# Performance work log

Measured on AMD Instinct MI355X. Metric: run time of the kernel, lower is better.

## Reference

```python
import jax, jax.numpy as jnp
import numpy as np

N_EMBD = 1024
N_HEAD = 16
HEAD_DIM = N_EMBD // N_HEAD


def setup_inputs() -> dict:
    key = jax.random.key(0)
    ks = jax.random.split(key, 8)
    B, T, T_ctx, C = 2, 2048, 2048, N_EMBD
    s = 1.0 / np.sqrt(C)
    return {
        "x": jax.random.normal(ks[0], (B, T, C), dtype=jnp.float32),
        "context": jax.random.normal(ks[1], (B, T_ctx, C), dtype=jnp.float32),
        # Linear weights stored as [in, out] (torch stores [out, in]; math identical via x @ W)
        "Wq": jax.random.normal(ks[2], (C, C), dtype=jnp.float32) * s,
        "bq": jnp.zeros((C,), dtype=jnp.float32),
        "Wkv": jax.random.normal(ks[3], (C, 2 * C), dtype=jnp.float32) * s,
        "bkv": jnp.zeros((2 * C,), dtype=jnp.float32),
        "Wp": jax.random.normal(ks[4], (C, C), dtype=jnp.float32) * s,
        "bp": jnp.zeros((C,), dtype=jnp.float32),
    }


def reference(x, context, Wq, bq, Wkv, bkv, Wp, bp):
    B, T, C = x.shape
    T_ctx = context.shape[1]
    H, D = N_HEAD, C // N_HEAD

    q = (x @ Wq + bq).reshape(B, T, H, D).transpose(0, 2, 1, 3)          # [B,H,T,D]
    kv = context @ Wkv + bkv                                             # [B,T_ctx,2C]
    k, v = jnp.split(kv, 2, axis=-1)
    k = k.reshape(B, T_ctx, H, D).transpose(0, 2, 1, 3)                  # [B,H,T_ctx,D]
    v = v.reshape(B, T_ctx, H, D).transpose(0, 2, 1, 3)                  # [B,H,T_ctx,D]

    att = jnp.einsum("bhtd,bhsd->bhts", q, k) * (1.0 / jnp.sqrt(jnp.asarray(D, q.dtype)))
    # tril(ones(T, T_ctx)): position t attends to context positions s <= t
    causal = jnp.arange(T)[:, None] >= jnp.arange(T_ctx)[None, :]        # [T,T_ctx]
    att = jnp.where(causal[None, None], att, jnp.asarray(-jnp.inf, att.dtype))
    att = jax.nn.softmax(att, axis=-1)

    y = jnp.einsum("bhts,bhsd->bhtd", att, v)                            # [B,H,T,D]
    y = y.transpose(0, 2, 1, 3).reshape(B, T, C)
    return y @ Wp + bp
```

## Files before the change

### kernel.cpp

```cpp
#include <hip/hip_runtime.h>
#include <hip/hip_bf16.h>

typedef __bf16 bf16;
typedef __bf16 bf16x8 __attribute__((ext_vector_type(8)));
typedef __bf16 bf16x4 __attribute__((ext_vector_type(4)));
typedef float f32x4 __attribute__((ext_vector_type(4)));
typedef float f32x16 __attribute__((ext_vector_type(16)));

#define GLOAD_LDS16(g, l) \
  __builtin_amdgcn_global_load_lds((const __attribute__((address_space(1))) void*)(g), \
                                   (__attribute__((address_space(3))) void*)(l), 16, 0, 0)

static __device__ __forceinline__ unsigned cvtpk_bf16(float lo, float hi) {
  unsigned r;
  asm("v_cvt_pk_bf16_f32 %0, %1, %2" : "=v"(r) : "v"(lo), "v"(hi));
  return r;
}
static __device__ __forceinline__ void pl32swap(unsigned& a, unsigned& b) {
  asm volatile("v_permlane32_swap_b32 %0, %1" : "+v"(a), "+v"(b));
}

__global__ __launch_bounds__(256) void prep_kernel(
    const float* __restrict__ x, const float* __restrict__ ctx,
    const float* __restrict__ Wq, const float* __restrict__ Wkv, const float* __restrict__ Wp,
    bf16* __restrict__ x_bf, bf16* __restrict__ c_bf,
    bf16* __restrict__ Wq_t, bf16* __restrict__ Wkv_t, bf16* __restrict__ Wp_t) {
  const int bid = blockIdx.x;
  const int tid = threadIdx.x;
  if (bid < 8192) {
    const int i = (bid & 4095) * 256 + tid;
    const float4 v = (bid < 4096) ? ((const float4*)x)[i] : ((const float4*)ctx)[i];
    bf16x4 o;
    o.x = (bf16)v.x; o.y = (bf16)v.y; o.z = (bf16)v.z; o.w = (bf16)v.w;
    if (bid < 4096) ((bf16x4*)x_bf)[i] = o; else ((bf16x4*)c_bf)[i] = o;
    return;
  }
  __shared__ float tile[128][33];
  int tb = bid - 8192;
  const float* W; bf16* Wt; int N, by, bx;
  if (tb < 256)       { W = Wq;  Wt = Wq_t;  N = 1024; by = tb >> 5; bx = tb & 31; }
  else if (tb < 768)  { tb -= 256; W = Wkv; Wt = Wkv_t; N = 2048; by = tb >> 6; bx = tb & 63; }
  else                { tb -= 768; W = Wp;  Wt = Wp_t;  N = 1024; by = tb >> 5; bx = tb & 31; }
  const int k0 = by * 128, n0 = bx * 32;
#pragma unroll
  for (int i = 0; i < 16; ++i) {
    const int idx = tid + i * 256;
    const int r = idx >> 5, c = idx & 31;
    tile[r][c] = W[(size_t)(k0 + r) * N + n0 + c];
  }
  __syncthreads();
#pragma unroll
  for (int p = 0; p < 2; ++p) {
    const int slot = tid + p * 256;
    const int n = slot >> 4, kg = slot & 15;
    bf16x8 v;
#pragma unroll
    for (int j = 0; j < 8; ++j) v[j] = (bf16)tile[kg * 8 + j][n];
    *(bf16x8*)(Wt + (size_t)(n0 + n) * 1024 + k0 + kg * 8) = v;
  }
}

__global__ __launch_bounds__(512) void proj_gemm_kernel(
    const bf16* __restrict__ x_bf, const bf16* __restrict__ c_bf,
    const bf16* __restrict__ Wq_t, const bf16* __restrict__ Wkv_t,
    const float* __restrict__ bq, const float* __restrict__ bkv,
    bf16* __restrict__ Qh, bf16* __restrict__ Kh, bf16* __restrict__ Vt) {
  __shared__ __align__(16) bf16 SM[24576];
  bf16* As = SM;
  bf16* Bs = SM + 16384;
  bf16* Vb = SM;

  const int tid = threadIdx.x;
  const int lane = tid & 63;
  const int w = tid >> 6;
  const int wm = w >> 2, wn = w & 3;
  const int g4 = lane >> 4, r16 = lane & 15;
  const int wu = __builtin_amdgcn_readfirstlane(w);

  int bid = blockIdx.x;
  bid = (bid & 7) * 48 + (bid >> 3);
  const bool isq = bid < 128;
  const int lid = isq ? bid : bid - 128;
  const int bx = isq ? (lid & 7) : (lid & 15);
  const int by = isq ? (lid >> 3) : (lid >> 4);
  const int m0 = by * 256, n0 = bx * 128;
  const bf16* A = isq ? x_bf : c_bf;
  const bf16* Bt = isq ? Wq_t : Wkv_t;
  const float* bias = isq ? bq : bkv;

  const bf16* Abase = A + (size_t)m0 * 1024;
  const bf16* Bbase = Bt + (size_t)n0 * 1024;
  int aoff[4], boff[2];
#pragma unroll
  for (int it = 0; it < 4; ++it) {
    const int s = it * 512 + tid;
    const int row = s >> 3, j = s & 7;
    aoff[it] = row * 1024 + (j ^ (row & 7)) * 8;
  }
#pragma unroll
  for (int it = 0; it < 2; ++it) {
    const int s = it * 512 + tid;
    const int row = s >> 3, j = s & 7;
    boff[it] = row * 1024 + (j ^ (row & 7)) * 8;
  }

  f32x4 acc[8][2] = {};

  for (int k0 = 0; k0 < 1024; k0 += 64) {
    __syncthreads();
#pragma unroll
    for (int it = 0; it < 4; ++it)
      GLOAD_LDS16(Abase + aoff[it] + k0, As + (it * 512 + wu * 64) * 8);
#pragma unroll
    for (int it = 0; it < 2; ++it)
      GLOAD_LDS16(Bbase + boff[it] + k0, Bs + (it * 512 + wu * 64) * 8);
    __syncthreads();
#pragma unroll
    for (int kk = 0; kk < 2; ++kk) {
      bf16x8 bfr[2];
#pragma unroll
      for (int ni = 0; ni < 2; ni++) {
        const int lr = wn * 32 + ni * 16 + r16;
        bfr[ni] = *(const bf16x8*)(Bs + lr * 64 + ((kk * 4 + g4) ^ (lr & 7)) * 8);
      }
#pragma unroll
      for (int mi = 0; mi < 8; mi++) {
        const int lr = wm * 128 + mi * 16 + r16;
        const bf16x8 a = *(const bf16x8*)(As + lr * 64 + ((kk * 4 + g4) ^ (lr & 7)) * 8);
        acc[mi][0] = __builtin_amdgcn_mfma_f32_16x16x32_bf16(a, bfr[0], acc[mi][0], 0, 0, 0);
        acc[mi][1] = __builtin_amdgcn_mfma_f32_16x16x32_bf16(a, bfr[1], acc[mi][1], 0, 0, 0);
      }
    }
  }

  if (!isq && n0 >= 1024) {
    const int bb = m0 >> 11, t0l = m0 & 2047;
#pragma unroll
    for (int p = 0; p < 2; ++p) {
      __syncthreads();
      if ((wn >> 1) == p) {
#pragma unroll
        for (int mi = 0; mi < 8; mi++)
#pragma unroll
          for (int ni = 0; ni < 2; ni++) {
            const int cl = (wn & 1) * 32 + ni * 16 + r16;
            const float bv = bias[n0 + p * 64 + cl];
#pragma unroll
            for (int r = 0; r < 4; r++) {
              const int rl = wm * 128 + mi * 16 + 4 * g4 + r;
              Vb[cl * 264 + rl] = (bf16)(acc[mi][ni][r] + bv);
            }
          }
      }
      __syncthreads();
      const int c2b = n0 - 1024 + p * 64;
#pragma unroll
      for (int pp = 0; pp < 4; ++pp) {
        const int slot = tid + pp * 512;
        const int d = slot >> 5, j = slot & 31;
        const int cc = c2b + d;
        const int h = cc >> 6, dd = cc & 63;
        *(bf16x8*)(Vt + ((size_t)((bb * 16 + h) * 64 + dd)) * 2048 + t0l + j * 8) =
            *(const bf16x8*)(Vb + d * 264 + j * 8);
      }
    }
    return;
  }

#pragma unroll
  for (int mi = 0; mi < 8; mi++) {
#pragma unroll
    for (int ni = 0; ni < 2; ni++) {
      const int col = n0 + wn * 32 + ni * 16 + r16;
      const float bv = bias[col];
      const int rowb = m0 + wm * 128 + mi * 16 + 4 * g4;
      const int h = col >> 6, d = col & 63;
#pragma unroll
      for (int r = 0; r < 4; r++) {
        const int row = rowb + r;
        const int bb = row >> 11, t = row & 2047;
        const float v = acc[mi][ni][r] + bv;
        if (isq)
          Qh[((size_t)(bb * 16 + h) * 2048 + t) * 64 + d] = (bf16)(v * 0.18033688f);
        else
          Kh[((size_t)(bb * 16 + h) * 2048 + t) * 64 + d] = (bf16)v;
      }
    }
  }
}

__global__ __launch_bounds__(256) void gemm_out_kernel(
    const bf16* __restrict__ A, const bf16* __restrict__ Bt,
    const float* __restrict__ bias, float* __restrict__ out) {
  __shared__ __align__(16) bf16 As[128 * 64];
  __shared__ __align__(16) bf16 Bs[64 * 64];

  const int tid = threadIdx.x;
  const int lane = tid & 63;
  const int w = tid >> 6;
  const int wr = w >> 1, wc = w & 1;
  const int g4 = lane >> 4, r16 = lane & 15;
  const int wu = __builtin_amdgcn_readfirstlane(w);

  int bid = blockIdx.x;
  bid = (bid & 7) * 64 + (bid >> 3);
  const int bx = bid & 15, by = bid >> 4;
  const int m0 = by * 128, n0 = bx * 64;

  const bf16* Abase = A + (size_t)m0 * 1024;
  const bf16* Bbase = Bt + (size_t)n0 * 1024;
  int aoff[4], boff[2];
#pragma unroll
  for (int it = 0; it < 4; ++it) {
    const int s = it * 256 + tid;
    const int row = s >> 3, j = s & 7;
    aoff[it] = row * 1024 + (j ^ (row & 7)) * 8;
  }
#pragma unroll
  for (int it = 0; it < 2; ++it) {
    const int s = it * 256 + tid;
    const int row = s >> 3, j = s & 7;
    boff[it] = row * 1024 + (j ^ (row & 7)) * 8;
  }

  f32x4 acc[4][2] = {};

  for (int k0 = 0; k0 < 1024; k0 += 64) {
    __syncthreads();
#pragma unroll
    for (int it = 0; it < 4; ++it)
      GLOAD_LDS16(Abase + aoff[it] + k0, As + (it * 256 + wu * 64) * 8);
#pragma unroll
    for (int it = 0; it < 2; ++it)
      GLOAD_LDS16(Bbase + boff[it] + k0, Bs + (it * 256 + wu * 64) * 8);
    __syncthreads();
#pragma unroll
    for (int kk = 0; kk < 2; ++kk) {
      bf16x8 af[4], bfr[2];
#pragma unroll
      for (int i = 0; i < 4; i++) {
        const int lr = wr * 64 + i * 16 + r16;
        af[i] = *(const bf16x8*)(As + lr * 64 + ((kk * 4 + g4) ^ (lr & 7)) * 8);
      }
#pragma unroll
      for (int i = 0; i < 2; i++) {
        const int lr = wc * 32 + i * 16 + r16;
        bfr[i] = *(const bf16x8*)(Bs + lr * 64 + ((kk * 4 + g4) ^ (lr & 7)) * 8);
      }
#pragma unroll
      for (int mi = 0; mi < 4; mi++)
#pragma unroll
        for (int ni = 0; ni < 2; ni++)
          acc[mi][ni] = __builtin_amdgcn_mfma_f32_16x16x32_bf16(af[mi], bfr[ni], acc[mi][ni], 0, 0, 0);
    }
  }

#pragma unroll
  for (int mi = 0; mi < 4; mi++)
#pragma unroll
    for (int ni = 0; ni < 2; ni++) {
      const int col = n0 + wc * 32 + ni * 16 + r16;
      const float bv = bias[col];
      const int rowb = m0 + wr * 64 + mi * 16 + 4 * g4;
#pragma unroll
      for (int r = 0; r < 4; r++)
        out[(size_t)(rowb + r) * 1024 + col] = acc[mi][ni][r] + bv;
    }
}

#define AE2(c, tb, te, sl) ((c) | ((tb) << 3) | ((te) << 9) | ((sl) << 15))
__constant__ int ATAB[12] = {
  AE2(7, 0, 16, 6), AE2(7, 16, 32, 7), AE2(3, 0, 16, 0),
  AE2(6, 0, 14, 4), AE2(6, 14, 28, 5), AE2(5, 0, 12, 2),
  AE2(5, 12, 24, 3), AE2(2, 0, 12, 0), AE2(4, 0, 10, 0),
  AE2(4, 10, 20, 1), AE2(1, 0, 8, 0),  AE2(0, 0, 4, 0),
};

__global__ __launch_bounds__(512) void attn_kernel(
    const bf16* __restrict__ Q, const bf16* __restrict__ Kh,
    const bf16* __restrict__ Vt, bf16* __restrict__ Y,
    bf16* __restrict__ Po, float* __restrict__ Lsum) {
  __shared__ __align__(16) bf16 Kls[2][4096];
  __shared__ __align__(16) bf16 Vls[2][4096];

  const int tid = threadIdx.x;
  const int lane = tid & 63;
  const int w = tid >> 6;
  const int l31 = lane & 31;
  const int g = lane >> 5;
  const int u = blockIdx.x >> 5;
  const int bh = blockIdx.x & 31;
  const int e = ATAB[u];
  const int c = e & 7, tb = (e >> 3) & 63, te = (e >> 9) & 63, slot = (e >> 15) & 7;
  const int slotg = bh * 8 + slot;
  const bool single = (tb == 0) && (te == 4 * c + 4);
  const int b = bh >> 4, h = bh & 15;
  const int qb = c * 256;
  const int wq = qb + w * 32;
  const int wu = __builtin_amdgcn_readfirstlane(w);

  bf16x8 qf[4];
  {
    const bf16* qp = Q + ((size_t)bh * 2048 + wq + l31) * 64 + g * 8;
#pragma unroll
    for (int cc = 0; cc < 4; ++cc) qf[cc] = *(const bf16x8*)(qp + cc * 16);
  }

  f32x16 O0 = {}, O1 = {};
  float l = 0.f;

  auto stage = [&](int bi, int s0) {
    const int s = tid >> 3, j = tid & 7;
    const int js = (j ^ (s & 7)) * 8;
    GLOAD_LDS16(Kh + ((size_t)bh * 2048 + s0 + s) * 64 + js, &Kls[bi][wu * 512]);
    GLOAD_LDS16(Vt + ((size_t)bh * 64 + s) * 2048 + s0 + js, &Vls[bi][wu * 512]);
  };

  stage(tb & 1, tb * 64);

  for (int t = tb; t < te; ++t) {
    const int s0 = t * 64;
    asm volatile("s_waitcnt vmcnt(0)" ::: "memory");
    __builtin_amdgcn_s_barrier();
    asm volatile("" ::: "memory");
    if (t + 1 < te) stage((t + 1) & 1, s0 + 64);

    if (s0 < wq + 32) {
      const bf16* Kb = Kls[t & 1];
      const bf16* Vb = Vls[t & 1];

      f32x16 SA = {}, SB = {};
      __builtin_amdgcn_s_setprio(1);
#pragma unroll
      for (int cc = 0; cc < 4; ++cc) {
        const int sl = ((cc * 2 + g) ^ (l31 & 7)) * 8;
        bf16x8 kf0 = *(const bf16x8*)(Kb + l31 * 64 + sl);
        SA = __builtin_amdgcn_mfma_f32_32x32x16_bf16(kf0, qf[cc], SA, 0, 0, 0);
        bf16x8 kf1 = *(const bf16x8*)(Kb + (32 + l31) * 64 + sl);
        SB = __builtin_amdgcn_mfma_f32_32x32x16_bf16(kf1, qf[cc], SB, 0, 0, 0);
      }
      __builtin_amdgcn_s_setprio(0);

      const int qg = wq + l31;
      if (s0 + 63 > wq) {
#pragma unroll
        for (int r = 0; r < 16; ++r) {
          const int sl = (r & 3) + 8 * (r >> 2) + 4 * g;
          SA[r] = (s0 + sl <= qg) ? SA[r] : -3.0e38f;
          SB[r] = (s0 + 32 + sl <= qg) ? SB[r] : -3.0e38f;
        }
      }

      float ps = 0.f;
#pragma unroll
      for (int r = 0; r < 16; ++r) { SA[r] = __builtin_amdgcn_exp2f(SA[r]); ps += SA[r]; }
#pragma unroll
      for (int r = 0; r < 16; ++r) { SB[r] = __builtin_amdgcn_exp2f(SB[r]); ps += SB[r]; }
      l += ps;

      union PW { unsigned u[4]; bf16x8 v; };
      PW pa0, pa1, pa2, pa3;
      {
        unsigned A0 = cvtpk_bf16(SA[0], SA[1]), B0 = cvtpk_bf16(SA[2], SA[3]);
        unsigned C0 = cvtpk_bf16(SA[4], SA[5]), D0 = cvtpk_bf16(SA[6], SA[7]);
        pl32swap(A0, C0); pl32swap(B0, D0);
        pa0.u[0] = A0; pa0.u[1] = B0; pa0.u[2] = C0; pa0.u[3] = D0;

        unsigned A1 = cvtpk_bf16(SA[8], SA[9]), B1 = cvtpk_bf16(SA[10], SA[11]);
        unsigned C1 = cvtpk_bf16(SA[12], SA[13]), D1 = cvtpk_bf16(SA[14], SA[15]);
        pl32swap(A1, C1); pl32swap(B1, D1);
        pa1.u[0] = A1; pa1.u[1] = B1; pa1.u[2] = C1; pa1.u[3] = D1;

        unsigned A2 = cvtpk_bf16(SB[0], SB[1]), B2 = cvtpk_bf16(SB[2], SB[3]);
        unsigned C2 = cvtpk_bf16(SB[4], SB[5]), D2 = cvtpk_bf16(SB[6], SB[7]);
        pl32swap(A2, C2); pl32swap(B2, D2);
        pa2.u[0] = A2; pa2.u[1] = B2; pa2.u[2] = C2; pa2.u[3] = D2;

        unsigned A3 = cvtpk_bf16(SB[8], SB[9]), B3 = cvtpk_bf16(SB[10], SB[11]);
        unsigned C3 = cvtpk_bf16(SB[12], SB[13]), D3 = cvtpk_bf16(SB[14], SB[15]);
        pl32swap(A3, C3); pl32swap(B3, D3);
        pa3.u[0] = A3; pa3.u[1] = B3; pa3.u[2] = C3; pa3.u[3] = D3;
      }

      __builtin_amdgcn_s_setprio(1);
#pragma unroll
      for (int cc = 0; cc < 4; ++cc) {
        const bf16x8 pav = (cc == 0) ? pa0.v : (cc == 1) ? pa1.v : (cc == 2) ? pa2.v : pa3.v;
        const int sl = ((cc * 2 + g) ^ (l31 & 7)) * 8;
        bf16x8 vf0 = *(const bf16x8*)(Vb + l31 * 64 + sl);
        O0 = __builtin_amdgcn_mfma_f32_32x32x16_bf16(pav, vf0, O0, 0, 0, 0);
        bf16x8 vf1 = *(const bf16x8*)(Vb + (32 + l31) * 64 + sl);
        O1 = __builtin_amdgcn_mfma_f32_32x32x16_bf16(pav, vf1, O1, 0, 0, 0);
      }
      __builtin_amdgcn_s_setprio(0);
    }
  }

  l += __shfl_xor(l, 32, 64);
  if (!single && g == 0)
    Lsum[(size_t)slotg * 256 + w * 32 + l31] = l;
#pragma unroll
  for (int r = 0; r < 16; ++r) {
    const int qr = (r & 3) + 8 * (r >> 2) + (g << 2);
    const float lr = __shfl(l, qr, 64);
    const float inv = (lr > 0.f) ? 1.f / lr : 0.f;
    if (single) {
      const int tq = wq + qr;
      bf16* yp = Y + ((size_t)(b * 2048 + tq)) * 1024 + h * 64 + l31;
      yp[0]  = (bf16)(O0[r] * inv);
      yp[32] = (bf16)(O1[r] * inv);
    } else {
      bf16* pp = Po + (size_t)slotg * 16384 + (w * 32 + qr) * 64 + l31;
      pp[0]  = (bf16)(O0[r] * inv);
      pp[32] = (bf16)(O1[r] * inv);
    }
  }
}

__global__ __launch_bounds__(256) void attn_combine(
    const bf16* __restrict__ Po, const float* __restrict__ Lsum, bf16* __restrict__ Y) {
  const int bh = blockIdx.x >> 2, ci = blockIdx.x & 3;
  const int c = ci + 4;
  const int base = bh * 8 + ci * 2;
  const int b = bh >> 4, h = bh & 15;
  const int tid = threadIdx.x;
#pragma unroll
  for (int k = 0; k < 8; ++k) {
    const int tt = tid + k * 256;
    const int row = tt >> 3, cg = tt & 7;
    const float w0 = Lsum[(size_t)base * 256 + row];
    const float w1 = Lsum[(size_t)(base + 1) * 256 + row];
    const bf16x8 v0 = *(const bf16x8*)(Po + (size_t)base * 16384 + row * 64 + cg * 8);
    const bf16x8 v1 = *(const bf16x8*)(Po + (size_t)(base + 1) * 16384 + row * 64 + cg * 8);
    const float inv = 1.f / (w0 + w1);
    bf16x8 o;
#pragma unroll
    for (int j = 0; j < 8; ++j) o[j] = (bf16)((w0 * (float)v0[j] + w1 * (float)v1[j]) * inv);
    const int t = c * 256 + row;
    *(bf16x8*)(Y + ((size_t)(b * 2048 + t)) * 1024 + h * 64 + cg * 8) = o;
  }
}

extern "C" void kernel_launch(void* const* d_in, const int* in_sizes, int n_in,
                              void* d_out, int out_size, void* d_ws, size_t ws_size,
                              hipStream_t stream) {
  (void)in_sizes; (void)n_in; (void)out_size; (void)ws_size;
  const float* x   = (const float*)d_in[0];
  const float* ctx = (const float*)d_in[1];
  const float* Wq  = (const float*)d_in[2];
  const float* bq  = (const float*)d_in[3];
  const float* Wkv = (const float*)d_in[4];
  const float* bkv = (const float*)d_in[5];
  const float* Wp  = (const float*)d_in[6];
  const float* bp  = (const float*)d_in[7];
  float* out = (float*)d_out;

  char* ws = (char*)d_ws;
  const size_t MB = 1024 * 1024;
  bf16*  Po    = (bf16*)(ws + 0 * MB);
  float* Lsum  = (float*)(ws + 9 * MB);
  bf16* x_bf   = (bf16*)(ws + 0 * MB);
  bf16* c_bf   = (bf16*)(ws + 10 * MB);
  bf16* Wq_t   = (bf16*)(ws + 18 * MB);
  bf16* Wkv_t  = (bf16*)(ws + 20 * MB);
  bf16* Wp_t   = (bf16*)(ws + 24 * MB);
  bf16* Qh     = (bf16*)(ws + 26 * MB);
  bf16* Kh     = (bf16*)(ws + 34 * MB);
  bf16* Vt     = (bf16*)(ws + 42 * MB);
  bf16* y_bf   = (bf16*)(ws + 50 * MB);

  prep_kernel<<<9216, 256, 0, stream>>>(x, ctx, Wq, Wkv, Wp, x_bf, c_bf, Wq_t, Wkv_t, Wp_t);
  proj_gemm_kernel<<<384, 512, 0, stream>>>(x_bf, c_bf, Wq_t, Wkv_t, bq, bkv, Qh, Kh, Vt);
  attn_kernel<<<384, 512, 0, stream>>>(Qh, Kh, Vt, y_bf, Po, Lsum);
  attn_combine<<<128, 256, 0, stream>>>(Po, Lsum, y_bf);
  gemm_out_kernel<<<512, 256, 0, stream>>>(y_bf, Wp_t, bp, out);
}
```

Measured before the change: 98.64 us.

## Fuse fp32-to-bf16 activation conversion into projection GEMM A-tile loads

```diff
diff --git a/kernel.cpp b/kernel.cpp
--- a/kernel.cpp
+++ b/kernel.cpp
@@ -21,22 +21,11 @@
 }
 
 __global__ __launch_bounds__(256) void prep_kernel(
-    const float* __restrict__ x, const float* __restrict__ ctx,
     const float* __restrict__ Wq, const float* __restrict__ Wkv, const float* __restrict__ Wp,
-    bf16* __restrict__ x_bf, bf16* __restrict__ c_bf,
     bf16* __restrict__ Wq_t, bf16* __restrict__ Wkv_t, bf16* __restrict__ Wp_t) {
-  const int bid = blockIdx.x;
   const int tid = threadIdx.x;
-  if (bid < 8192) {
-    const int i = (bid & 4095) * 256 + tid;
-    const float4 v = (bid < 4096) ? ((const float4*)x)[i] : ((const float4*)ctx)[i];
-    bf16x4 o;
-    o.x = (bf16)v.x; o.y = (bf16)v.y; o.z = (bf16)v.z; o.w = (bf16)v.w;
-    if (bid < 4096) ((bf16x4*)x_bf)[i] = o; else ((bf16x4*)c_bf)[i] = o;
-    return;
-  }
   __shared__ float tile[128][33];
-  int tb = bid - 8192;
+  int tb = blockIdx.x;
   const float* W; bf16* Wt; int N, by, bx;
   if (tb < 256)       { W = Wq;  Wt = Wq_t;  N = 1024; by = tb >> 5; bx = tb & 31; }
   else if (tb < 768)  { tb -= 256; W = Wkv; Wt = Wkv_t; N = 2048; by = tb >> 6; bx = tb & 63; }
@@ -61,7 +50,7 @@
 }
 
 __global__ __launch_bounds__(512) void proj_gemm_kernel(
-    const bf16* __restrict__ x_bf, const bf16* __restrict__ c_bf,
+    const float* __restrict__ x, const float* __restrict__ ctx,
     const bf16* __restrict__ Wq_t, const bf16* __restrict__ Wkv_t,
     const float* __restrict__ bq, const float* __restrict__ bkv,
     bf16* __restrict__ Qh, bf16* __restrict__ Kh, bf16* __restrict__ Vt) {
@@ -84,19 +73,13 @@
   const int bx = isq ? (lid & 7) : (lid & 15);
   const int by = isq ? (lid >> 3) : (lid >> 4);
   const int m0 = by * 256, n0 = bx * 128;
-  const bf16* A = isq ? x_bf : c_bf;
+  const float* Af = isq ? x : ctx;
   const bf16* Bt = isq ? Wq_t : Wkv_t;
   const float* bias = isq ? bq : bkv;
 
-  const bf16* Abase = A + (size_t)m0 * 1024;
+  const float* Abase = Af + (size_t)m0 * 1024;
   const bf16* Bbase = Bt + (size_t)n0 * 1024;
-  int aoff[4], boff[2];
-#pragma unroll
-  for (int it = 0; it < 4; ++it) {
-    const int s = it * 512 + tid;
-    const int row = s >> 3, j = s & 7;
-    aoff[it] = row * 1024 + (j ^ (row & 7)) * 8;
-  }
+  int boff[2];
 #pragma unroll
   for (int it = 0; it < 2; ++it) {
     const int s = it * 512 + tid;
@@ -104,17 +87,47 @@
     boff[it] = row * 1024 + (j ^ (row & 7)) * 8;
   }
 
+  float4 areg[8];
+  auto issueA = [&](int k0) {
+#pragma unroll
+    for (int it = 0; it < 8; ++it) {
+      const int s = it * 512 + tid;
+      const int row = s >> 4, c4 = s & 15;
+      areg[it] = *(const float4*)(Abase + (size_t)row * 1024 + k0 + c4 * 4);
+    }
+  };
+  auto writeA = [&]() {
+#pragma unroll
+    for (int it = 0; it < 8; ++it) {
+      const int s = it * 512 + tid;
+      const int row = s >> 4, c4 = s & 15;
+      uint2 pv;
+      pv.x = cvtpk_bf16(areg[it].x, areg[it].y);
+      pv.y = cvtpk_bf16(areg[it].z, areg[it].w);
+      *(uint2*)(As + row * 64 + (((c4 >> 1) ^ (row & 7)) * 8) + (c4 & 1) * 4) = pv;
+    }
+  };
+
   f32x4 acc[8][2] = {};
 
-  for (int k0 = 0; k0 < 1024; k0 += 64) {
-    __syncthreads();
-#pragma unroll
-    for (int it = 0; it < 4; ++it)
-      GLOAD_LDS16(Abase + aoff[it] + k0, As + (it * 512 + wu * 64) * 8);
+  issueA(0);
+  for (int kt = 0; kt < 16; ++kt) {
+    const int k0 = kt * 64;
+    __builtin_amdgcn_s_barrier();
+    asm volatile("" ::: "memory");
+    writeA();
 #pragma unroll
     for (int it = 0; it < 2; ++it)
       GLOAD_LDS16(Bbase + boff[it] + k0, Bs + (it * 512 + wu * 64) * 8);
-    __syncthreads();
+    if (kt + 1 < 16) {
+      issueA(k0 + 64);
+      asm volatile("s_waitcnt vmcnt(8) lgkmcnt(0)" ::: "memory");
+    } else {
+      asm volatile("s_waitcnt vmcnt(0) lgkmcnt(0)" ::: "memory");
+    }
+    __builtin_amdgcn_s_barrier();
+    __builtin_amdgcn_sched_barrier(0);
+    asm volatile("" ::: "memory");
 #pragma unroll
     for (int kk = 0; kk < 2; ++kk) {
       bf16x8 bfr[2];
@@ -123,6 +136,7 @@
         const int lr = wn * 32 + ni * 16 + r16;
         bfr[ni] = *(const bf16x8*)(Bs + lr * 64 + ((kk * 4 + g4) ^ (lr & 7)) * 8);
       }
+      __builtin_amdgcn_s_setprio(1);
 #pragma unroll
       for (int mi = 0; mi < 8; mi++) {
         const int lr = wm * 128 + mi * 16 + r16;
@@ -130,6 +144,7 @@
         acc[mi][0] = __builtin_amdgcn_mfma_f32_16x16x32_bf16(a, bfr[0], acc[mi][0], 0, 0, 0);
         acc[mi][1] = __builtin_amdgcn_mfma_f32_16x16x32_bf16(a, bfr[1], acc[mi][1], 0, 0, 0);
       }
+      __builtin_amdgcn_s_setprio(0);
     }
   }
 
@@ -459,8 +474,6 @@
   const size_t MB = 1024 * 1024;
   bf16*  Po    = (bf16*)(ws + 0 * MB);
   float* Lsum  = (float*)(ws + 9 * MB);
-  bf16* x_bf   = (bf16*)(ws + 0 * MB);
-  bf16* c_bf   = (bf16*)(ws + 10 * MB);
   bf16* Wq_t   = (bf16*)(ws + 18 * MB);
   bf16* Wkv_t  = (bf16*)(ws + 20 * MB);
   bf16* Wp_t   = (bf16*)(ws + 24 * MB);
@@ -469,8 +482,8 @@
   bf16* Vt     = (bf16*)(ws + 42 * MB);
   bf16* y_bf   = (bf16*)(ws + 50 * MB);
 
-  prep_kernel<<<9216, 256, 0, stream>>>(x, ctx, Wq, Wkv, Wp, x_bf, c_bf, Wq_t, Wkv_t, Wp_t);
-  proj_gemm_kernel<<<384, 512, 0, stream>>>(x_bf, c_bf, Wq_t, Wkv_t, bq, bkv, Qh, Kh, Vt);
+  prep_kernel<<<1024, 256, 0, stream>>>(Wq, Wkv, Wp, Wq_t, Wkv_t, Wp_t);
+  proj_gemm_kernel<<<384, 512, 0, stream>>>(x, ctx, Wq_t, Wkv_t, bq, bkv, Qh, Kh, Vt);
   attn_kernel<<<384, 512, 0, stream>>>(Qh, Kh, Vt, y_bf, Po, Lsum);
   attn_combine<<<128, 256, 0, stream>>>(Po, Lsum, y_bf);
   gemm_out_kernel<<<512, 256, 0, stream>>>(y_bf, Wp_t, bp, out);
```

After: 115.1 us (median of 2 runs). 1.17x slower.
